# Kernel optimization log

Measured on AMD Instinct MI355X. Metric: run time of the kernel, lower is better.

The kernel has to match this reference:

```python
import jax, jax.numpy as jnp
import numpy as np

N_NODES = 100000
DIN = 512
B = 1024
T_STEPS = 6
DOUT = 512


def setup_inputs() -> dict:
    key = jax.random.key(0)
    ks = jax.random.split(key, 8)
    s = 0.02  # small init scale for numerical sanity
    x = jax.random.normal(ks[0], (N_NODES, DIN), jnp.float32)
    batch = jnp.sort(jax.random.randint(ks[1], (N_NODES,), 0, B)).astype(jnp.int64)
    Wih = jax.random.normal(ks[2], (4 * DIN, 2 * DIN), jnp.float32) * s
    Whh = jax.random.normal(ks[3], (4 * DIN, DIN), jnp.float32) * s
    bih = jax.random.normal(ks[4], (4 * DIN,), jnp.float32) * s
    bhh = jax.random.normal(ks[5], (4 * DIN,), jnp.float32) * s
    Wpost = jax.random.normal(ks[6], (DOUT, 2 * DIN), jnp.float32) * s
    bpost = jax.random.normal(ks[7], (DOUT,), jnp.float32) * s
    return {"x": x, "batch": batch, "Wih": Wih, "Whh": Whh, "bih": bih,
            "bhh": bhh, "Wpost": Wpost, "bpost": bpost, "num_graphs": B}


def reference(x, batch, Wih, Whh, bih, bhh, Wpost, bpost, num_graphs):
    din = x.shape[1]
    Bg = num_graphs
    h = jnp.zeros((Bg, din), x.dtype)
    c = jnp.zeros((Bg, din), x.dtype)
    q_star = jnp.zeros((Bg, 2 * din), x.dtype)  # [q, r]
    for _ in range(T_STEPS):
        # single-layer LSTM cell over the "batch of graphs" axis
        z = q_star @ Wih.T + h @ Whh.T + (bih + bhh)  # [B, 4*din]
        i, f, g, o = jnp.split(z, 4, axis=-1)  # torch gate order i,f,g,o
        c = jax.nn.sigmoid(f) * c + jax.nn.sigmoid(i) * jnp.tanh(g)
        h = jax.nn.sigmoid(o) * jnp.tanh(c)
        q = h  # [B, din]
        # segment (scatter) softmax attention over nodes of each graph
        e = jnp.sum(x * q[batch], axis=-1)  # [N]
        emax = jax.ops.segment_max(e, batch, num_segments=Bg)
        ex = jnp.exp(e - emax[batch])
        denom = jax.ops.segment_sum(ex, batch, num_segments=Bg)
        a = ex / denom[batch]  # [N]
        r = jax.ops.segment_sum(a[:, None] * x, batch, num_segments=Bg)  # [B, din]
        q_star = jnp.concatenate([q, r], axis=-1)
    # post_pool: Linear(2*din -> dim_out) + bias + ReLU (dropout=0, eval mode)
    out = jax.nn.relu(q_star @ Wpost.T + bpost)
    return out
```

## Files before the change

### kernel.cpp

```cpp
#include <hip/hip_runtime.h>
#include <stdint.h>
#include <stddef.h>

#define DIN    512
#define BGR    1024
#define NGATE  2048
#define KQ     1024
#define DOUT   512
#define TSTEPS 6

typedef unsigned short ushort_t;
typedef short bf16x8 __attribute__((ext_vector_type(8)));
typedef unsigned short u16x8 __attribute__((ext_vector_type(8)));
typedef float f32x4 __attribute__((ext_vector_type(4)));

__device__ __forceinline__ float b2f(unsigned short u) {
    unsigned int i = ((unsigned int)u) << 16;
    float f;
    __builtin_memcpy(&f, &i, 4);
    return f;
}

__device__ __forceinline__ unsigned short f2b(float f) {
    unsigned int i;
    __builtin_memcpy(&i, &f, 4);
    unsigned int lsb = (i >> 16) & 1u;
    i += 0x7fffu + lsb;
    return (unsigned short)(i >> 16);
}

__device__ __forceinline__ float fast_sigmoid(float v) {
    return 1.f / (1.f + __expf(-v));
}

__device__ __forceinline__ float fast_tanh(float v) {
    float t = fabsf(v);
    float e = __expf(-2.f * t);
    float r = (1.f - e) / (1.f + e);
    return v < 0.f ? -r : r;
}

__device__ __forceinline__ void gld_lds16(const ushort_t* g, ushort_t* l) {
    auto const* gp = reinterpret_cast<const unsigned int __attribute__((address_space(1)))*>(
        reinterpret_cast<uintptr_t>(g));
    auto* lp = reinterpret_cast<unsigned int __attribute__((address_space(3)))*>(
        reinterpret_cast<uintptr_t>(l));
    __builtin_amdgcn_global_load_lds(gp, lp, 16, 0, 0);
}

#define BM 64
#define BN 64
#define BK 32

__global__ __launch_bounds__(256)
void gemm_cell(const ushort_t* __restrict__ Ag,
               const ushort_t* __restrict__ Wg,
               const float* __restrict__ bias2,
               float* __restrict__ c, float* __restrict__ H)
{
    __shared__ __align__(16) ushort_t As[64 * 64];
    __shared__ __align__(16) ushort_t Bs[64 * 64];

    const int tid  = threadIdx.x;
    const int lane = tid & 63;
    const int w    = tid >> 6;
    const int lrow = lane & 15;
    const int quad = lane >> 4;

    const int n0 = blockIdx.x * 64;
    const int m0 = blockIdx.y * 64;

    const int r8  = lane >> 3;
    const int csw = 8 * ((lane & 7) ^ r8);

    const ushort_t* aS0 = Ag + (size_t)(m0 + w * 16 + r8) * KQ + csw;
    const ushort_t* aS1 = Ag + (size_t)(m0 + w * 16 + 8 + r8) * KQ + csw;
    const ushort_t* bS0 = Wg + (size_t)(n0 + w * 16 + r8) * KQ + csw;
    const ushort_t* bS1 = Wg + (size_t)(n0 + w * 16 + 8 + r8) * KQ + csw;
    ushort_t* aL0 = As + w * 1024;
    ushort_t* aL1 = As + w * 1024 + 512;
    ushort_t* bL0 = Bs + w * 1024;
    ushort_t* bL1 = Bs + w * 1024 + 512;

    f32x4 acc4[4];
#pragma unroll
    for (int ni = 0; ni < 4; ni++) acc4[ni] = (f32x4){0.f, 0.f, 0.f, 0.f};

    const int rx = lrow & 7;

    for (int kt = 0; kt < KQ; kt += 64) {
        __syncthreads();
        gld_lds16(aS0 + kt, aL0);
        gld_lds16(aS1 + kt, aL1);
        gld_lds16(bS0 + kt, bL0);
        gld_lds16(bS1 + kt, bL1);
        __syncthreads();

#pragma unroll
        for (int ks = 0; ks < 2; ks++) {
            const int coff = 8 * ((ks * 4 + quad) ^ rx);
            bf16x8 af = *(const bf16x8*)&As[(w * 16 + lrow) * 64 + coff];
            bf16x8 bfr[4];
#pragma unroll
            for (int ni = 0; ni < 4; ni++)
                bfr[ni] = *(const bf16x8*)&Bs[(ni * 16 + lrow) * 64 + coff];
#pragma unroll
            for (int ni = 0; ni < 4; ni++)
                acc4[ni] = __builtin_amdgcn_mfma_f32_16x16x32_bf16(
                    af, bfr[ni], acc4[ni], 0, 0, 0);
        }
    }

    const int dd  = blockIdx.x * 16 + lrow;
    const float bi_ = bias2[n0 + lrow];
    const float bf_ = bias2[n0 + 16 + lrow];
    const float bg_ = bias2[n0 + 32 + lrow];
    const float bo_ = bias2[n0 + 48 + lrow];
#pragma unroll
    for (int r = 0; r < 4; r++) {
        const int gm = m0 + w * 16 + quad * 4 + r;
        float zi = acc4[0][r] + bi_;
        float zf = acc4[1][r] + bf_;
        float zg = acc4[2][r] + bg_;
        float zo = acc4[3][r] + bo_;
        size_t off = (size_t)gm * DIN + dd;
        float cc = c[off];
        cc = fast_sigmoid(zf) * cc + fast_sigmoid(zi) * fast_tanh(zg);
        float hh = fast_sigmoid(zo) * fast_tanh(cc);
        c[off] = cc;
        H[off] = hh;
    }
}

template <int MODE>
__global__ __launch_bounds__(256)
void gemm_bt(const ushort_t* __restrict__ Ag, const ushort_t* __restrict__ Bgm,
             const float* __restrict__ bias, float* __restrict__ Cout,
             int M, int N, int K)
{
    __shared__ __align__(16) ushort_t As[BM * BK];
    __shared__ __align__(16) ushort_t Bs[BN * BK];

    const int tid  = threadIdx.x;
    const int lane = tid & 63;
    const int w    = tid >> 6;
    const int wr   = w >> 1;
    const int wc   = w & 1;
    const int lrow = lane & 15;
    const int quad = lane >> 4;

    const int n0 = blockIdx.x * BN;
    const int m0 = blockIdx.y * BM;

    const int srow = tid >> 2;
    const int scol = (tid & 3) * 8;

    const ushort_t* aSrc = Ag  + (size_t)(m0 + srow) * K + scol;
    const ushort_t* bSrc = Bgm + (size_t)(n0 + srow) * K + scol;

    f32x4 acc[2][2];
#pragma unroll
    for (int i = 0; i < 2; i++)
#pragma unroll
        for (int j = 0; j < 2; j++)
            acc[i][j] = (f32x4){0.f, 0.f, 0.f, 0.f};

    bf16x8 av = *(const bf16x8*)(aSrc);
    bf16x8 bv = *(const bf16x8*)(bSrc);

    for (int kt = 0; kt < K; kt += BK) {
        __syncthreads();
        *(bf16x8*)&As[srow * BK + scol] = av;
        *(bf16x8*)&Bs[srow * BK + scol] = bv;
        if (kt + BK < K) {
            av = *(const bf16x8*)(aSrc + kt + BK);
            bv = *(const bf16x8*)(bSrc + kt + BK);
        }
        __syncthreads();

        bf16x8 af[2], bfr[2];
#pragma unroll
        for (int mi = 0; mi < 2; mi++)
            af[mi] = *(const bf16x8*)&As[(wr * 32 + mi * 16 + lrow) * BK + quad * 8];
#pragma unroll
        for (int ni = 0; ni < 2; ni++)
            bfr[ni] = *(const bf16x8*)&Bs[(wc * 32 + ni * 16 + lrow) * BK + quad * 8];

#pragma unroll
        for (int mi = 0; mi < 2; mi++)
#pragma unroll
            for (int ni = 0; ni < 2; ni++)
                acc[mi][ni] = __builtin_amdgcn_mfma_f32_16x16x32_bf16(
                    af[mi], bfr[ni], acc[mi][ni], 0, 0, 0);
    }

#pragma unroll
    for (int mi = 0; mi < 2; mi++) {
#pragma unroll
        for (int ni = 0; ni < 2; ni++) {
#pragma unroll
            for (int r = 0; r < 4; r++) {
                int gm = m0 + wr * 32 + mi * 16 + quad * 4 + r;
                int gn = n0 + wc * 32 + ni * 16 + lrow;
                float v = acc[mi][ni][r] + bias[gn];
                if (MODE == 1) {
                    if (!(v > 0.f) && (v == v)) v = 0.f;
                }
                Cout[(size_t)gm * N + gn] = v;
            }
        }
    }
}

template <int XMODE>
__global__ __launch_bounds__(256, 4)
void attn_step(const ushort_t* __restrict__ xbsrc, const ushort_t* __restrict__ xraw,
               ushort_t* __restrict__ xbdst, const int* __restrict__ offs,
               const float* __restrict__ H, ushort_t* __restrict__ A,
               const int* __restrict__ flags)
{
    const int b    = blockIdx.x;
    const int tid  = threadIdx.x;
    const int lane = tid & 63;
    const int w    = tid >> 6;
    const int xf   = (XMODE == 0) ? 0 : flags[0];

    __shared__ float accL[4][DIN];
    __shared__ float mw[4], lw[4];

    const float* hrow = H + (size_t)b * DIN;
    {
        const int dq = tid * 2;
        unsigned int qw = (unsigned int)f2b(hrow[dq])
                        | ((unsigned int)f2b(hrow[dq + 1]) << 16);
        *(unsigned int*)&A[(size_t)b * KQ + dq] = qw;
    }
    f32x4 q0v = *(const f32x4*)(hrow + lane * 8);
    f32x4 q1v = *(const f32x4*)(hrow + lane * 8 + 4);
    float q8[8] = {q0v[0], q0v[1], q0v[2], q0v[3], q1v[0], q1v[1], q1v[2], q1v[3]};

    const int s  = offs[b];
    const int en = offs[b + 1];

    const float NEG_INF = -__builtin_inff();
    float m = NEG_INF, l = 0.f;
    float acc[8];
#pragma unroll
    for (int j = 0; j < 8; j++) acc[j] = 0.f;

    auto load_row = [&](int n, float* v) {
        if (XMODE == 0 || !xf) {
            const ushort_t* src = (XMODE == 0) ? xbsrc : xraw;
            u16x8 xv = *(const u16x8*)(src + (size_t)n * DIN + lane * 8);
#pragma unroll
            for (int j = 0; j < 8; j++) v[j] = b2f(xv[j]);
            if (XMODE == 1)
                *(u16x8*)(xbdst + (size_t)n * DIN + lane * 8) = xv;
        } else {
            const float* xp = (const float*)xraw;
            f32x4 v0 = *(const f32x4*)(xp + (size_t)n * DIN + lane * 8);
            f32x4 v1 = *(const f32x4*)(xp + (size_t)n * DIN + lane * 8 + 4);
#pragma unroll
            for (int j = 0; j < 4; j++) { v[j] = v0[j]; v[4 + j] = v1[j]; }
            if (XMODE == 1) {
                u16x8 o;
#pragma unroll
                for (int j = 0; j < 8; j++) o[j] = f2b(v[j]);
                *(u16x8*)(xbdst + (size_t)n * DIN + lane * 8) = o;
            }
        }
    };

    auto update = [&](float e, const float* xv) {
        float mn = fmaxf(m, e);
        float al = __expf(m - mn);
        float pp = __expf(e - mn);
        l = l * al + pp;
#pragma unroll
        for (int j = 0; j < 8; j++) acc[j] = acc[j] * al + pp * xv[j];
        m = mn;
    };

    float x0[8] = {0.f}, x1[8] = {0.f}, x2[8] = {0.f}, x3[8] = {0.f};
    int n = s + w;
    if (n < en)      load_row(n, x0);
    if (n + 4 < en)  load_row(n + 4, x1);
    if (n + 8 < en)  load_row(n + 8, x2);
    if (n + 12 < en) load_row(n + 12, x3);
    for (; n < en; n += 16) {
        float p0[8], p1[8], p2[8], p3[8];
        const int np = n + 16;
        if (np < en)      load_row(np, p0);
        if (np + 4 < en)  load_row(np + 4, p1);
        if (np + 8 < en)  load_row(np + 8, p2);
        if (np + 12 < en) load_row(np + 12, p3);

        float e0 = 0.f, e1 = 0.f, e2 = 0.f, e3 = 0.f;
#pragma unroll
        for (int j = 0; j < 8; j++) {
            e0 += q8[j] * x0[j];
            e1 += q8[j] * x1[j];
            e2 += q8[j] * x2[j];
            e3 += q8[j] * x3[j];
        }
#pragma unroll
        for (int off = 32; off > 0; off >>= 1) {
            e0 += __shfl_xor(e0, off, 64);
            e1 += __shfl_xor(e1, off, 64);
            e2 += __shfl_xor(e2, off, 64);
            e3 += __shfl_xor(e3, off, 64);
        }

        update(e0, x0);
        if (n + 4 < en)  update(e1, x1);
        if (n + 8 < en)  update(e2, x2);
        if (n + 12 < en) update(e3, x3);

#pragma unroll
        for (int j = 0; j < 8; j++) {
            x0[j] = p0[j]; x1[j] = p1[j]; x2[j] = p2[j]; x3[j] = p3[j];
        }
    }

    if (lane == 0) { mw[w] = m; lw[w] = l; }
#pragma unroll
    for (int j = 0; j < 8; j++) accL[w][lane * 8 + j] = acc[j];
    __syncthreads();

    const float M = fmaxf(fmaxf(mw[0], mw[1]), fmaxf(mw[2], mw[3]));
    const int d0 = tid * 2;
    float r0 = 0.f, r1 = 0.f, lt = 0.f;
#pragma unroll
    for (int ww = 0; ww < 4; ww++) {
        float mwv = mw[ww];
        float a = (mwv == NEG_INF) ? 0.f : __expf(mwv - M);
        lt += a * lw[ww];
        r0 += a * accL[ww][d0];
        r1 += a * accL[ww][d0 + 1];
    }
    float inv = lt > 0.f ? 1.f / lt : 0.f;
    unsigned int rw = (unsigned int)f2b(r0 * inv)
                    | ((unsigned int)f2b(r1 * inv) << 16);
    *(unsigned int*)&A[(size_t)b * KQ + DIN + d0] = rw;
}

__global__ void prep_all(const ushort_t* __restrict__ x,
                         const ushort_t* __restrict__ Wih,
                         const ushort_t* __restrict__ Whh,
                         const ushort_t* __restrict__ bih,
                         const ushort_t* __restrict__ bhh,
                         const ushort_t* __restrict__ Wpost,
                         const ushort_t* __restrict__ bpost,
                         const int* __restrict__ batch, int Nn,
                         ushort_t* __restrict__ Wp,
                         float* __restrict__ bias2,
                         float* __restrict__ biaspost,
                         ushort_t* __restrict__ Wpb,
                         float* __restrict__ c,
                         float* __restrict__ H,
                         ushort_t* __restrict__ A,
                         int* __restrict__ offs,
                         int* __restrict__ flags)
{
    __shared__ int cnt[7];
    __shared__ int fsh[7];
    const int tid = threadIdx.x;
    if (tid < 7) cnt[tid] = 0;
    __syncthreads();
    {
        const int t = tid >> 5;
        const int l = tid & 31;
        if (t < 7) {
            const ushort_t* pp = (t == 0) ? x : (t == 1) ? Wih : (t == 2) ? Whh
                               : (t == 3) ? bih : (t == 4) ? bhh
                               : (t == 5) ? Wpost : bpost;
            int good = 0;
            for (int i = 0; i < 4; i++) {
                ushort_t u = pp[(l * 4 + i) * 2];
                int ex = (u >> 7) & 0xFF;
                if (ex == 0 || (ex >= 96 && ex <= 143)) good++;
            }
            atomicAdd(&cnt[t], good);
        }
    }
    __syncthreads();
    if (tid < 7) fsh[tid] = (cnt[tid] < 96) ? 1 : 0;
    __syncthreads();
    const int fWih = fsh[1], fWhh = fsh[2], fbih = fsh[3];
    const int fbhh = fsh[4], fWpo = fsh[5], fbpo = fsh[6];

    const int idx = blockIdx.x * 256 + tid;
    if (blockIdx.x == 0 && tid < 7) flags[tid] = fsh[tid];

    if (idx < NGATE * KQ) {
        const int nn = idx >> 10;
        const int k  = idx & 1023;
        const int g  = (nn >> 4) & 3;
        const int n  = g * 512 + (nn >> 6) * 16 + (nn & 15);
        const int widx = n * KQ + k;
        float v = fWih ? ((const float*)Wih)[widx] : b2f(Wih[widx]);
        if (k < DIN) {
            int hidx = n * DIN + k;
            v += fWhh ? ((const float*)Whh)[hidx] : b2f(Whh[hidx]);
        }
        Wp[idx] = f2b(v);
    }
    if (idx < DOUT * KQ) {
        Wpb[idx] = fWpo ? f2b(((const float*)Wpost)[idx]) : Wpost[idx];
    }
    if (idx < NGATE) {
        const int g = (idx >> 4) & 3;
        const int n = g * 512 + (idx >> 6) * 16 + (idx & 15);
        float v1 = fbih ? ((const float*)bih)[n] : b2f(bih[n]);
        float v2 = fbhh ? ((const float*)bhh)[n] : b2f(bhh[n]);
        bias2[idx] = v1 + v2;
    }
    if (idx < DOUT) {
        biaspost[idx] = fbpo ? ((const float*)bpost)[idx] : b2f(bpost[idx]);
    }

    if (idx < BGR * DIN) {
        const int d = idx & (DIN - 1);
        float zi = fbih ? ((const float*)bih)[d] : b2f(bih[d]);
        zi      += fbhh ? ((const float*)bhh)[d] : b2f(bhh[d]);
        float zg = fbih ? ((const float*)bih)[2 * DIN + d] : b2f(bih[2 * DIN + d]);
        zg      += fbhh ? ((const float*)bhh)[2 * DIN + d] : b2f(bhh[2 * DIN + d]);
        float zo = fbih ? ((const float*)bih)[3 * DIN + d] : b2f(bih[3 * DIN + d]);
        zo      += fbhh ? ((const float*)bhh)[3 * DIN + d] : b2f(bhh[3 * DIN + d]);
        float c0 = fast_sigmoid(zi) * fast_tanh(zg);
        float h0 = fast_sigmoid(zo) * fast_tanh(c0);
        c[idx] = c0;
        H[idx] = h0;
        const int bg = idx >> 9;
        A[(size_t)bg * KQ + d]       = f2b(h0);
        A[(size_t)bg * KQ + DIN + d] = 0;
    }

    if (idx < Nn) {
        const bool is64 = batch[Nn - 1] < batch[Nn - 2];
        int cur  = is64 ? batch[2 * idx] : batch[idx];
        int prev = (idx == 0) ? -1 : (is64 ? batch[2 * (idx - 1)] : batch[idx - 1]);
        for (int bb = prev + 1; bb <= cur; ++bb) offs[bb] = idx;
        if (idx == Nn - 1) {
            for (int bb = cur + 1; bb <= BGR; ++bb) offs[bb] = Nn;
        }
    }
}

extern "C" void kernel_launch(void* const* d_in, const int* in_sizes, int n_in,
                              void* d_out, int out_size, void* d_ws, size_t ws_size,
                              hipStream_t stream)
{
    const ushort_t* x     = (const ushort_t*)d_in[0];
    const int*      batch = (const int*)d_in[1];
    const ushort_t* Wih   = (const ushort_t*)d_in[2];
    const ushort_t* Whh   = (const ushort_t*)d_in[3];
    const ushort_t* bih   = (const ushort_t*)d_in[4];
    const ushort_t* bhh   = (const ushort_t*)d_in[5];
    const ushort_t* Wpost = (const ushort_t*)d_in[6];
    const ushort_t* bpost = (const ushort_t*)d_in[7];
    const int Nn = in_sizes[1];
    const long long Tx = (long long)in_sizes[0];

    char* p = (char*)d_ws;
    auto carve = [&](size_t bytes) -> void* {
        char* q = p;
        p += (bytes + 255) & ~(size_t)255;
        return (void*)q;
    };
    ushort_t* Wp       = (ushort_t*)carve((size_t)NGATE * KQ * 2);
    ushort_t* Wpb      = (ushort_t*)carve((size_t)DOUT * KQ * 2);
    float*    bias2    = (float*)carve((size_t)NGATE * 4);
    float*    biaspost = (float*)carve((size_t)DOUT * 4);
    float*    c        = (float*)carve((size_t)BGR * DIN * 4);
    float*    H        = (float*)carve((size_t)BGR * DIN * 4);
    ushort_t* A        = (ushort_t*)carve((size_t)BGR * KQ * 2);
    int*      offs     = (int*)carve((size_t)(BGR + 1) * 4);
    int*      flags    = (int*)carve(16 * 4);
    size_t used = (size_t)(p - (char*)d_ws);
    const bool use_xb = (ws_size >= used + (size_t)Tx * 2 + 256);
    ushort_t* xb = use_xb ? (ushort_t*)carve((size_t)Tx * 2) : nullptr;

    prep_all<<<(NGATE * KQ) / 256, 256, 0, stream>>>(
        x, Wih, Whh, bih, bhh, Wpost, bpost, batch, Nn,
        Wp, bias2, biaspost, Wpb, c, H, A, offs, flags);

    for (int t = 0; t < TSTEPS; ++t) {
        if (t > 0)
            gemm_cell<<<dim3(NGATE / 64, BGR / 64), 256, 0, stream>>>(
                A, Wp, bias2, c, H);
        if (use_xb) {
            if (t == 0)
                attn_step<1><<<BGR, 256, 0, stream>>>(xb, x, xb, offs, H, A, flags);
            else
                attn_step<0><<<BGR, 256, 0, stream>>>(xb, x, xb, offs, H, A, flags);
        } else {
            attn_step<2><<<BGR, 256, 0, stream>>>(x, x, nullptr, offs, H, A, flags);
        }
    }
    gemm_bt<1><<<dim3(DOUT / BN, BGR / BM), 256, 0, stream>>>(
        A, Wpb, biaspost, (float*)d_out, BGR, DOUT, KQ);
}
```

Before: 530.6 us.

## Retile LSTM cell GEMM to 2x2 warps and split attention rows across half-waves

The LSTM gate GEMM now uses a 2x2 warp grid with 32x32 warp tiles and register-prefetched global loads, replacing the direct global-to-LDS loads and swizzle. Because of this tiling the g/o gates land in other warps, so they are exchanged through a shared-memory epilogue buffer. The attention kernel now assigns each node row to a 32-lane half-wave with 16 elements per lane, giving 8 row groups per block and a shorter shuffle reduction. Intended costs removed are per-warp MFMA fragment reloads and reduction overhead, traded for LDS bank conflicts from dropping the swizzle, an extra sync, and higher register pressure.

```diff
diff --git a/kernel.cpp b/kernel.cpp
--- a/kernel.cpp
+++ b/kernel.cpp
@@ -39,18 +39,6 @@
     float r = (1.f - e) / (1.f + e);
     return v < 0.f ? -r : r;
 }
-
-__device__ __forceinline__ void gld_lds16(const ushort_t* g, ushort_t* l) {
-    auto const* gp = reinterpret_cast<const unsigned int __attribute__((address_space(1)))*>(
-        reinterpret_cast<uintptr_t>(g));
-    auto* lp = reinterpret_cast<unsigned int __attribute__((address_space(3)))*>(
-        reinterpret_cast<uintptr_t>(l));
-    __builtin_amdgcn_global_load_lds(gp, lp, 16, 0, 0);
-}
-
-#define BM 64
-#define BN 64
-#define BK 32
 
 __global__ __launch_bounds__(256)
 void gemm_cell(const ushort_t* __restrict__ Ag,
@@ -60,77 +48,111 @@
 {
     __shared__ __align__(16) ushort_t As[64 * 64];
     __shared__ __align__(16) ushort_t Bs[64 * 64];
+    __shared__ float Ep[2][2][32][16];
 
     const int tid  = threadIdx.x;
     const int lane = tid & 63;
     const int w    = tid >> 6;
+    const int wr   = w >> 1;
+    const int wc   = w & 1;
     const int lrow = lane & 15;
     const int quad = lane >> 4;
 
     const int n0 = blockIdx.x * 64;
     const int m0 = blockIdx.y * 64;
 
-    const int r8  = lane >> 3;
-    const int csw = 8 * ((lane & 7) ^ r8);
-
-    const ushort_t* aS0 = Ag + (size_t)(m0 + w * 16 + r8) * KQ + csw;
-    const ushort_t* aS1 = Ag + (size_t)(m0 + w * 16 + 8 + r8) * KQ + csw;
-    const ushort_t* bS0 = Wg + (size_t)(n0 + w * 16 + r8) * KQ + csw;
-    const ushort_t* bS1 = Wg + (size_t)(n0 + w * 16 + 8 + r8) * KQ + csw;
-    ushort_t* aL0 = As + w * 1024;
-    ushort_t* aL1 = As + w * 1024 + 512;
-    ushort_t* bL0 = Bs + w * 1024;
-    ushort_t* bL1 = Bs + w * 1024 + 512;
-
-    f32x4 acc4[4];
-#pragma unroll
-    for (int ni = 0; ni < 4; ni++) acc4[ni] = (f32x4){0.f, 0.f, 0.f, 0.f};
-
-    const int rx = lrow & 7;
+    const int srow = tid >> 3;
+    const int scol = (tid & 7) * 8;
+
+    const ushort_t* aSrc = Ag + (size_t)(m0 + srow) * KQ + scol;
+    const ushort_t* bSrc = Wg + (size_t)(n0 + srow) * KQ + scol;
+    const size_t half = (size_t)32 * KQ;
+
+    f32x4 acc[2][2];
+#pragma unroll
+    for (int i = 0; i < 2; i++)
+#pragma unroll
+        for (int j = 0; j < 2; j++)
+            acc[i][j] = (f32x4){0.f, 0.f, 0.f, 0.f};
+
+    bf16x8 av0 = *(const bf16x8*)(aSrc);
+    bf16x8 av1 = *(const bf16x8*)(aSrc + half);
+    bf16x8 bv0 = *(const bf16x8*)(bSrc);
+    bf16x8 bv1 = *(const bf16x8*)(bSrc + half);
 
     for (int kt = 0; kt < KQ; kt += 64) {
         __syncthreads();
-        gld_lds16(aS0 + kt, aL0);
-        gld_lds16(aS1 + kt, aL1);
-        gld_lds16(bS0 + kt, bL0);
-        gld_lds16(bS1 + kt, bL1);
+        *(bf16x8*)&As[srow * 64 + scol]        = av0;
+        *(bf16x8*)&As[(srow + 32) * 64 + scol] = av1;
+        *(bf16x8*)&Bs[srow * 64 + scol]        = bv0;
+        *(bf16x8*)&Bs[(srow + 32) * 64 + scol] = bv1;
+        if (kt + 64 < KQ) {
+            av0 = *(const bf16x8*)(aSrc + kt + 64);
+            av1 = *(const bf16x8*)(aSrc + half + kt + 64);
+            bv0 = *(const bf16x8*)(bSrc + kt + 64);
+            bv1 = *(const bf16x8*)(bSrc + half + kt + 64);
+        }
         __syncthreads();
 
 #pragma unroll
         for (int ks = 0; ks < 2; ks++) {
-            const int coff = 8 * ((ks * 4 + quad) ^ rx);
-            bf16x8 af = *(const bf16x8*)&As[(w * 16 + lrow) * 64 + coff];
-            bf16x8 bfr[4];
-#pragma unroll
-            for (int ni = 0; ni < 4; ni++)
-                bfr[ni] = *(const bf16x8*)&Bs[(ni * 16 + lrow) * 64 + coff];
-#pragma unroll
-            for (int ni = 0; ni < 4; ni++)
-                acc4[ni] = __builtin_amdgcn_mfma_f32_16x16x32_bf16(
-                    af, bfr[ni], acc4[ni], 0, 0, 0);
-        }
-    }
-
-    const int dd  = blockIdx.x * 16 + lrow;
-    const float bi_ = bias2[n0 + lrow];
-    const float bf_ = bias2[n0 + 16 + lrow];
-    const float bg_ = bias2[n0 + 32 + lrow];
-    const float bo_ = bias2[n0 + 48 + lrow];
-#pragma unroll
-    for (int r = 0; r < 4; r++) {
-        const int gm = m0 + w * 16 + quad * 4 + r;
-        float zi = acc4[0][r] + bi_;
-        float zf = acc4[1][r] + bf_;
-        float zg = acc4[2][r] + bg_;
-        float zo = acc4[3][r] + bo_;
-        size_t off = (size_t)gm * DIN + dd;
-        float cc = c[off];
-        cc = fast_sigmoid(zf) * cc + fast_sigmoid(zi) * fast_tanh(zg);
-        float hh = fast_sigmoid(zo) * fast_tanh(cc);
-        c[off] = cc;
-        H[off] = hh;
-    }
-}
+            const int g8 = (ks * 4 + quad) * 8;
+            bf16x8 af[2], bfr[2];
+#pragma unroll
+            for (int mi = 0; mi < 2; mi++)
+                af[mi] = *(const bf16x8*)&As[(wr * 32 + mi * 16 + lrow) * 64 + g8];
+#pragma unroll
+            for (int ni = 0; ni < 2; ni++)
+                bfr[ni] = *(const bf16x8*)&Bs[(wc * 32 + ni * 16 + lrow) * 64 + g8];
+#pragma unroll
+            for (int mi = 0; mi < 2; mi++)
+#pragma unroll
+                for (int ni = 0; ni < 2; ni++)
+                    acc[mi][ni] = __builtin_amdgcn_mfma_f32_16x16x32_bf16(
+                        af[mi], bfr[ni], acc[mi][ni], 0, 0, 0);
+        }
+    }
+
+    if (wc == 1) {
+#pragma unroll
+        for (int mi = 0; mi < 2; mi++)
+#pragma unroll
+            for (int ni = 0; ni < 2; ni++)
+#pragma unroll
+                for (int r = 0; r < 4; r++)
+                    Ep[wr][ni][mi * 16 + quad * 4 + r][lrow] = acc[mi][ni][r];
+    }
+    __syncthreads();
+    if (wc == 0) {
+        const int dd  = blockIdx.x * 16 + lrow;
+        const float bi_ = bias2[n0 + lrow];
+        const float bf_ = bias2[n0 + 16 + lrow];
+        const float bg_ = bias2[n0 + 32 + lrow];
+        const float bo_ = bias2[n0 + 48 + lrow];
+#pragma unroll
+        for (int mi = 0; mi < 2; mi++) {
+#pragma unroll
+            for (int r = 0; r < 4; r++) {
+                const int rl = mi * 16 + quad * 4 + r;
+                const int gm = m0 + wr * 32 + rl;
+                float zi = acc[mi][0][r] + bi_;
+                float zf = acc[mi][1][r] + bf_;
+                float zg = Ep[wr][0][rl][lrow] + bg_;
+                float zo = Ep[wr][1][rl][lrow] + bo_;
+                size_t off = (size_t)gm * DIN + dd;
+                float cc = c[off];
+                cc = fast_sigmoid(zf) * cc + fast_sigmoid(zi) * fast_tanh(zg);
+                float hh = fast_sigmoid(zo) * fast_tanh(cc);
+                c[off] = cc;
+                H[off] = hh;
+            }
+        }
+    }
+}
+
+#define BM 64
+#define BN 64
+#define BK 32
 
 template <int MODE>
 __global__ __launch_bounds__(256)
@@ -221,12 +243,12 @@
 {
     const int b    = blockIdx.x;
     const int tid  = threadIdx.x;
-    const int lane = tid & 63;
-    const int w    = tid >> 6;
+    const int hg   = tid >> 5;
+    const int lh   = tid & 31;
     const int xf   = (XMODE == 0) ? 0 : flags[0];
 
-    __shared__ float accL[4][DIN];
-    __shared__ float mw[4], lw[4];
+    __shared__ float accL[8][DIN];
+    __shared__ float mw[8], lw[8];
 
     const float* hrow = H + (size_t)b * DIN;
     {
@@ -235,38 +257,51 @@
                         | ((unsigned int)f2b(hrow[dq + 1]) << 16);
         *(unsigned int*)&A[(size_t)b * KQ + dq] = qw;
     }
-    f32x4 q0v = *(const f32x4*)(hrow + lane * 8);
-    f32x4 q1v = *(const f32x4*)(hrow + lane * 8 + 4);
-    float q8[8] = {q0v[0], q0v[1], q0v[2], q0v[3], q1v[0], q1v[1], q1v[2], q1v[3]};
+    float q16[16];
+    {
+        const float* qp = hrow + lh * 16;
+#pragma unroll
+        for (int v4 = 0; v4 < 4; v4++) {
+            f32x4 qv = *(const f32x4*)(qp + v4 * 4);
+#pragma unroll
+            for (int j = 0; j < 4; j++) q16[v4 * 4 + j] = qv[j];
+        }
+    }
 
     const int s  = offs[b];
     const int en = offs[b + 1];
 
     const float NEG_INF = -__builtin_inff();
     float m = NEG_INF, l = 0.f;
-    float acc[8];
-#pragma unroll
-    for (int j = 0; j < 8; j++) acc[j] = 0.f;
+    float acc[16];
+#pragma unroll
+    for (int j = 0; j < 16; j++) acc[j] = 0.f;
 
     auto load_row = [&](int n, float* v) {
         if (XMODE == 0 || !xf) {
             const ushort_t* src = (XMODE == 0) ? xbsrc : xraw;
-            u16x8 xv = *(const u16x8*)(src + (size_t)n * DIN + lane * 8);
-#pragma unroll
-            for (int j = 0; j < 8; j++) v[j] = b2f(xv[j]);
-            if (XMODE == 1)
-                *(u16x8*)(xbdst + (size_t)n * DIN + lane * 8) = xv;
+            u16x8 x0 = *(const u16x8*)(src + (size_t)n * DIN + lh * 16);
+            u16x8 x1 = *(const u16x8*)(src + (size_t)n * DIN + lh * 16 + 8);
+#pragma unroll
+            for (int j = 0; j < 8; j++) { v[j] = b2f(x0[j]); v[8 + j] = b2f(x1[j]); }
+            if (XMODE == 1) {
+                *(u16x8*)(xbdst + (size_t)n * DIN + lh * 16)     = x0;
+                *(u16x8*)(xbdst + (size_t)n * DIN + lh * 16 + 8) = x1;
+            }
         } else {
-            const float* xp = (const float*)xraw;
-            f32x4 v0 = *(const f32x4*)(xp + (size_t)n * DIN + lane * 8);
-            f32x4 v1 = *(const f32x4*)(xp + (size_t)n * DIN + lane * 8 + 4);
-#pragma unroll
-            for (int j = 0; j < 4; j++) { v[j] = v0[j]; v[4 + j] = v1[j]; }
+            const float* xp = (const float*)xraw + (size_t)n * DIN + lh * 16;
+#pragma unroll
+            for (int v4 = 0; v4 < 4; v4++) {
+                f32x4 xv = *(const f32x4*)(xp + v4 * 4);
+#pragma unroll
+                for (int j = 0; j < 4; j++) v[v4 * 4 + j] = xv[j];
+            }
             if (XMODE == 1) {
-                u16x8 o;
-#pragma unroll
-                for (int j = 0; j < 8; j++) o[j] = f2b(v[j]);
-                *(u16x8*)(xbdst + (size_t)n * DIN + lane * 8) = o;
+                u16x8 o0, o1;
+#pragma unroll
+                for (int j = 0; j < 8; j++) { o0[j] = f2b(v[j]); o1[j] = f2b(v[8 + j]); }
+                *(u16x8*)(xbdst + (size_t)n * DIN + lh * 16)     = o0;
+                *(u16x8*)(xbdst + (size_t)n * DIN + lh * 16 + 8) = o1;
             }
         }
     };
@@ -277,66 +312,53 @@
         float pp = __expf(e - mn);
         l = l * al + pp;
 #pragma unroll
-        for (int j = 0; j < 8; j++) acc[j] = acc[j] * al + pp * xv[j];
+        for (int j = 0; j < 16; j++) acc[j] = acc[j] * al + pp * xv[j];
         m = mn;
     };
 
-    float x0[8] = {0.f}, x1[8] = {0.f}, x2[8] = {0.f}, x3[8] = {0.f};
-    int n = s + w;
-    if (n < en)      load_row(n, x0);
-    if (n + 4 < en)  load_row(n + 4, x1);
-    if (n + 8 < en)  load_row(n + 8, x2);
-    if (n + 12 < en) load_row(n + 12, x3);
+    float xa[16] = {0.f}, xc[16] = {0.f};
+    int n = s + hg;
+    if (n < en)     load_row(n, xa);
+    if (n + 8 < en) load_row(n + 8, xc);
     for (; n < en; n += 16) {
-        float p0[8], p1[8], p2[8], p3[8];
+        float pa[16], pc[16];
         const int np = n + 16;
-        if (np < en)      load_row(np, p0);
-        if (np + 4 < en)  load_row(np + 4, p1);
-        if (np + 8 < en)  load_row(np + 8, p2);
-        if (np + 12 < en) load_row(np + 12, p3);
-
-        float e0 = 0.f, e1 = 0.f, e2 = 0.f, e3 = 0.f;
-#pragma unroll
-        for (int j = 0; j < 8; j++) {
-            e0 += q8[j] * x0[j];
-            e1 += q8[j] * x1[j];
-            e2 += q8[j] * x2[j];
-            e3 += q8[j] * x3[j];
-        }
-#pragma unroll
-        for (int off = 32; off > 0; off >>= 1) {
-            e0 += __shfl_xor(e0, off, 64);
+        if (np < en)     load_row(np, pa);
+        if (np + 8 < en) load_row(np + 8, pc);
+
+        float e1 = 0.f, e2 = 0.f;
+#pragma unroll
+        for (int j = 0; j < 16; j++) { e1 += q16[j] * xa[j]; e2 += q16[j] * xc[j]; }
+#pragma unroll
+        for (int off = 16; off > 0; off >>= 1) {
             e1 += __shfl_xor(e1, off, 64);
             e2 += __shfl_xor(e2, off, 64);
-            e3 += __shfl_xor(e3, off, 64);
-        }
-
-        update(e0, x0);
-        if (n + 4 < en)  update(e1, x1);
-        if (n + 8 < en)  update(e2, x2);
-        if (n + 12 < en) update(e3, x3);
-
-#pragma unroll
-        for (int j = 0; j < 8; j++) {
-            x0[j] = p0[j]; x1[j] = p1[j]; x2[j] = p2[j]; x3[j] = p3[j];
-        }
-    }
-
-    if (lane == 0) { mw[w] = m; lw[w] = l; }
-#pragma unroll
-    for (int j = 0; j < 8; j++) accL[w][lane * 8 + j] = acc[j];
+        }
+
+        update(e1, xa);
+        if (n + 8 < en) update(e2, xc);
+
+#pragma unroll
+        for (int j = 0; j < 16; j++) { xa[j] = pa[j]; xc[j] = pc[j]; }
+    }
+
+    if (lh == 0) { mw[hg] = m; lw[hg] = l; }
+#pragma unroll
+    for (int j = 0; j < 16; j++) accL[hg][lh * 16 + j] = acc[j];
     __syncthreads();
 
-    const float M = fmaxf(fmaxf(mw[0], mw[1]), fmaxf(mw[2], mw[3]));
+    float M = mw[0];
+#pragma unroll
+    for (int hh = 1; hh < 8; hh++) M = fmaxf(M, mw[hh]);
     const int d0 = tid * 2;
     float r0 = 0.f, r1 = 0.f, lt = 0.f;
 #pragma unroll
-    for (int ww = 0; ww < 4; ww++) {
-        float mwv = mw[ww];
+    for (int hh = 0; hh < 8; hh++) {
+        float mwv = mw[hh];
         float a = (mwv == NEG_INF) ? 0.f : __expf(mwv - M);
-        lt += a * lw[ww];
-        r0 += a * accL[ww][d0];
-        r1 += a * accL[ww][d0 + 1];
+        lt += a * lw[hh];
+        r0 += a * accL[hh][d0];
+        r1 += a * accL[hh][d0 + 1];
     }
     float inv = lt > 0.f ? 1.f / lt : 0.f;
     unsigned int rw = (unsigned int)f2b(r0 * inv)
```

Result: no change. 528.5 us (-0.4%).
